# Kernel optimization log

Measured on AMD Instinct MI355X. Metric: run time of the kernel, lower is better.

## Reference

```python
import jax, jax.numpy as jnp
import numpy as np
import math

IN_DIM, OUT_DIM, NUM_BASIS = 256, 128, 6
MAX_IN_SEQ, MAX_OUT_SEQ = 512, 256
REDUCTION = 2
LN_EPS = 1e-5


def setup_inputs() -> dict:
    key = jax.random.key(0)
    ks = jax.random.split(key, 8)
    u = lambda k, shape, a: jax.random.uniform(k, shape, jnp.float32, -a, a)
    x = jax.random.normal(ks[0], (16, MAX_IN_SEQ, IN_DIM), jnp.float32)
    M = u(ks[1], (OUT_DIM, IN_DIM), 0.5)
    P = u(ks[2], (OUT_DIM, OUT_DIM, NUM_BASIS), 0.1)
    Linker = u(ks[3], (MAX_IN_SEQ, MAX_OUT_SEQ), 0.1)
    ln_gamma = jnp.ones((OUT_DIM,), jnp.float32)
    ln_beta = jnp.zeros((OUT_DIM,), jnp.float32)
    res_W = u(ks[4], (OUT_DIM, IN_DIM), 0.1)
    res_linker = u(ks[5], (MAX_IN_SEQ, MAX_OUT_SEQ), 0.1)
    # periods[i,j,g] = i*(out_dim*num_basis) + j*num_basis + g + 2 (non-trainable buffer)
    periods = (jnp.arange(OUT_DIM * OUT_DIM * NUM_BASIS, dtype=jnp.float32)
               .reshape(OUT_DIM, OUT_DIM, NUM_BASIS) + 2.0)
    return {"x": x, "M": M, "P": P, "Linker": Linker, "ln_gamma": ln_gamma,
            "ln_beta": ln_beta, "res_W": res_W, "res_linker": res_linker,
            "periods": periods, "actual_seq_len": 512}


def _layer_norm(z, gamma, beta):
    mu = jnp.mean(z, axis=-1, keepdims=True)
    var = jnp.var(z, axis=-1, keepdims=True)
    return (z - mu) * jax.lax.rsqrt(var + LN_EPS) * gamma + beta


def reference(x, M, P, Linker, ln_gamma, ln_beta, res_W, res_linker, periods, actual_seq_len):
    b, seq_len, _ = x.shape
    # Z = LN(x @ M^T)
    Z = _layer_norm(jnp.matmul(x, M.T), ln_gamma, ln_beta)  # (b, s, out)
    # position-dependent trig basis: phi[s,i,j,g] = cos(2*pi*s / periods[i,j,g])
    k = jnp.arange(seq_len, dtype=jnp.float32)[:, None, None, None]
    phi = jnp.cos(2.0 * math.pi * k / periods[None])          # (s, out, out, nb)
    # fold basis into per-position mixing matrix, then contract (matches sum over dims 3,4)
    W = jnp.einsum('ijg,sijg->sij', P, phi)                   # (s, out, out)
    T = jnp.einsum('bsj,sij->bsi', Z, W)                      # (b, s, out)
    # adaptive linker: reduce sequence length
    L = actual_seq_len
    Lo = max(1, L // REDUCTION)
    U = jnp.einsum('bsi,so->boi', T[:, :L], Linker[:L, :Lo])  # (b, out_seq, out)
    # 'separate' residual
    rfeat = jnp.matmul(x[:, :L], res_W.T)                     # (b, s, out)
    residual = jnp.einsum('bsi,so->boi', rfeat, res_linker[:L, :Lo])
    return U + residual
```

## Files before the change

kernel.cpp:

```cpp
#include <hip/hip_runtime.h>
#include <hip/hip_bf16.h>

#define LN_EPS 1e-5f


typedef __attribute__((ext_vector_type(8))) short short8;
typedef __attribute__((ext_vector_type(4))) float floatx4;

__device__ __forceinline__ unsigned short f2bf(float f) {
    __hip_bfloat16 h = __float2bfloat16(f);
    union { __hip_bfloat16 h; unsigned short u; } v; v.h = h; return v.u;
}
__device__ __forceinline__ unsigned int pack2(float a, float b) {
    return (unsigned int)f2bf(a) | ((unsigned int)f2bf(b) << 16);
}
__device__ __forceinline__ short8 pack8(float4 a, float4 b) {
    union { short8 s; uint4 u; } v;
    v.u.x = pack2(a.x, a.y); v.u.y = pack2(a.z, a.w);
    v.u.z = pack2(b.x, b.y); v.u.w = pack2(b.z, b.w);
    return v.s;
}

union SMem {
    struct { float buf[32 * 258]; float red1[256]; float red2[256]; float mus[32]; float rsg[32]; } p1;
    unsigned short lcat[32 * 260];
};

__global__ __launch_bounds__(256) void s1_produce(const float* __restrict__ x,
                                                  const float* __restrict__ M,
                                                  const float* __restrict__ resW,
                                                  const float* __restrict__ gamma,
                                                  const float* __restrict__ beta,
                                                  const float* __restrict__ P,
                                                  const float* __restrict__ periods,
                                                  const float* __restrict__ Linker,
                                                  const float* __restrict__ resL,
                                                  unsigned short* __restrict__ Z,
                                                  unsigned short* __restrict__ TRt,
                                                  unsigned short* __restrict__ W,
                                                  unsigned short* __restrict__ LcatT) {
    __shared__ SMem sm;
    int blk = blockIdx.x, t = threadIdx.x;
    int w = t >> 6, l = t & 63;
    int lane15 = l & 15, quad = l >> 4;

    if (blk < 512) {
        int et = blk & 31, sc = blk >> 5;
        int n0 = et * 512 + t * 2;
        int jj = n0 & 7, ii = (n0 >> 3) & 127, qd = (n0 >> 10) & 3, kq = n0 >> 12;
        int e0 = ii * 128 + kq * 32 + qd * 8 + jj;
        const float* pp = P + (size_t)e0 * 6;
        float4 pa = *(const float4*)(pp);
        float4 pb = *(const float4*)(pp + 4);
        float4 pc = *(const float4*)(pp + 8);
        float pf[12] = { pa.x, pa.y, pa.z, pa.w, pb.x, pb.y, pb.z, pb.w, pc.x, pc.y, pc.z, pc.w };
        const float* qp = periods + (size_t)e0 * 6;
        float4 qa = *(const float4*)(qp);
        float4 qb = *(const float4*)(qp + 4);
        float4 qc = *(const float4*)(qp + 8);
        float iv[12] = { __builtin_amdgcn_rcpf(qa.x), __builtin_amdgcn_rcpf(qa.y),
                         __builtin_amdgcn_rcpf(qa.z), __builtin_amdgcn_rcpf(qa.w),
                         __builtin_amdgcn_rcpf(qb.x), __builtin_amdgcn_rcpf(qb.y),
                         __builtin_amdgcn_rcpf(qb.z), __builtin_amdgcn_rcpf(qb.w),
                         __builtin_amdgcn_rcpf(qc.x), __builtin_amdgcn_rcpf(qc.y),
                         __builtin_amdgcn_rcpf(qc.z), __builtin_amdgcn_rcpf(qc.w) };
        float s0f = (float)(sc * 32);
        float tc[12], cm1[12], cc[12];
        #pragma unroll
        for (int g = 0; g < 12; ++g) {
            tc[g]  = 2.0f * __builtin_amdgcn_cosf(iv[g]);
            cm1[g] = __builtin_amdgcn_cosf(__builtin_amdgcn_fractf(s0f * iv[g]));
            cc[g]  = __builtin_amdgcn_cosf(__builtin_amdgcn_fractf((s0f + 1.0f) * iv[g]));
        }
        #pragma unroll 4
        for (int ss = 0; ss < 32; ++ss) {
            float a0 = 0.f, a1 = 0.f;
            #pragma unroll
            for (int g = 0; g < 6; ++g)  a0 += pf[g] * cm1[g];
            #pragma unroll
            for (int g = 6; g < 12; ++g) a1 += pf[g] * cm1[g];
            int s = sc * 32 + ss;
            *(unsigned int*)(W + (size_t)s * 16384 + n0) = pack2(a0, a1);
            #pragma unroll
            for (int g = 0; g < 12; ++g) {
                float cn = fmaf(tc[g], cc[g], -cm1[g]);
                cm1[g] = cc[g]; cc[g] = cn;
            }
        }
    } else if (blk < 768) {
        int r0 = (blk - 512) * 32;
        const float* wbase = (w < 2) ? M : resW;
        int wco = (w < 2) ? (w * 64) : (w * 64 - 128);
        floatx4 acc[2][4] = {};
        for (int kk = 0; kk < 256; kk += 32) {
            int k0 = kk + quad * 8;
            const float* xr0 = x + (size_t)(r0 + lane15) * 256 + k0;
            const float* xr1 = x + (size_t)(r0 + 16 + lane15) * 256 + k0;
            short8 a0 = pack8(*(const float4*)xr0, *(const float4*)(xr0 + 4));
            short8 a1 = pack8(*(const float4*)xr1, *(const float4*)(xr1 + 4));
            #pragma unroll
            for (int nt = 0; nt < 4; ++nt) {
                const float* br = wbase + (size_t)(wco + nt * 16 + lane15) * 256 + k0;
                short8 b = pack8(*(const float4*)br, *(const float4*)(br + 4));
                acc[0][nt] = __builtin_amdgcn_mfma_f32_16x16x32_bf16(a0, b, acc[0][nt], 0, 0, 0);
                acc[1][nt] = __builtin_amdgcn_mfma_f32_16x16x32_bf16(a1, b, acc[1][nt], 0, 0, 0);
            }
        }
        #pragma unroll
        for (int mt = 0; mt < 2; ++mt)
            #pragma unroll
            for (int nt = 0; nt < 4; ++nt)
                #pragma unroll
                for (int r = 0; r < 4; ++r) {
                    int ro = mt * 16 + quad * 4 + r;
                    int co = w * 64 + nt * 16 + lane15;
                    sm.p1.buf[ro * 258 + co] = acc[mt][nt][r];
                }
        __syncthreads();
        {
            int r = t >> 3, seg = t & 7;
            float s1 = 0.f, s2 = 0.f;
            #pragma unroll
            for (int e = 0; e < 16; ++e) { float v = sm.p1.buf[r * 258 + seg * 16 + e]; s1 += v; s2 += v * v; }
            sm.p1.red1[r * 8 + seg] = s1; sm.p1.red2[r * 8 + seg] = s2;
        }
        __syncthreads();
        if (t < 32) {
            float s1 = 0.f, s2 = 0.f;
            #pragma unroll
            for (int e = 0; e < 8; ++e) { s1 += sm.p1.red1[t * 8 + e]; s2 += sm.p1.red2[t * 8 + e]; }
            float mu = s1 * (1.0f / 128.0f);
            float var = s2 * (1.0f / 128.0f) - mu * mu;
            sm.p1.mus[t] = mu; sm.p1.rsg[t] = rsqrtf(var + LN_EPS);
        }
        __syncthreads();
        int b = r0 >> 9, s0 = r0 & 511;
        {
            int r = t >> 3, c0 = (t & 7) * 16;
            int s_t = s0 + r;
            float mu = sm.p1.mus[r], rs = sm.p1.rsg[r];
            float zv[16];
            #pragma unroll
            for (int e = 0; e < 16; ++e) {
                int j = c0 + e;
                zv[e] = (sm.p1.buf[r * 258 + j] - mu) * rs * gamma[j] + beta[j];
            }
            uint4 oz0, oz1;
            oz0.x = pack2(zv[0], zv[1]);  oz0.y = pack2(zv[2], zv[3]);
            oz0.z = pack2(zv[4], zv[5]);  oz0.w = pack2(zv[6], zv[7]);
            oz1.x = pack2(zv[8], zv[9]);  oz1.y = pack2(zv[10], zv[11]);
            oz1.z = pack2(zv[12], zv[13]); oz1.w = pack2(zv[14], zv[15]);
            unsigned short* zdst = Z + (size_t)s_t * 2048 + (((c0 >> 3) * 16 + b) << 3);
            *(uint4*)(zdst) = oz0;
            *(uint4*)(zdst + 128) = oz1;
        }
        {
            int j = t >> 1, sh = (t & 1) * 16;
            unsigned int ow[8];
            #pragma unroll
            for (int p = 0; p < 8; ++p) {
                float v0 = sm.p1.buf[(sh + 2 * p) * 258 + 128 + j];
                float v1 = sm.p1.buf[(sh + 2 * p + 1) * 258 + 128 + j];
                ow[p] = pack2(v0, v1);
            }
            int kqA = 64 + ((s0 + sh) >> 3);
            unsigned short* dst = TRt + (size_t)b * 131072 + ((size_t)(kqA * 128 + j) << 3);
            uint4 u0; u0.x = ow[0]; u0.y = ow[1]; u0.z = ow[2]; u0.w = ow[3];
            uint4 u1; u1.x = ow[4]; u1.y = ow[5]; u1.z = ow[6]; u1.w = ow[7];
            *(uint4*)(dst) = u0;
            *(uint4*)(dst + 1024) = u1;
        }
    } else {
        int kb = blk - 768;
        int k0 = kb * 32;
        const float* src = (kb < 16) ? (Linker + (size_t)k0 * 256)
                                     : (resL + (size_t)(k0 - 512) * 256);
        #pragma unroll
        for (int q = 0; q < 8; ++q) {
            int lin = t + 256 * q;
            int row = lin >> 6, col4 = (lin & 63) * 4;
            float4 v = *(const float4*)(src + row * 256 + col4);
            *(unsigned int*)(sm.lcat + row * 260 + col4)     = pack2(v.x, v.y);
            *(unsigned int*)(sm.lcat + row * 260 + col4 + 2) = pack2(v.z, v.w);
        }
        __syncthreads();
        int o = t;
        unsigned int outw[16];
        #pragma unroll
        for (int kp = 0; kp < 16; ++kp) {
            unsigned int lo = sm.lcat[(2 * kp) * 260 + o];
            unsigned int hi = sm.lcat[(2 * kp + 1) * 260 + o];
            outw[kp] = lo | (hi << 16);
        }
        #pragma unroll
        for (int qq = 0; qq < 4; ++qq) {
            uint4 u; u.x = outw[qq*4]; u.y = outw[qq*4+1]; u.z = outw[qq*4+2]; u.w = outw[qq*4+3];
            *(uint4*)(LcatT + (((size_t)(kb * 4 + qq) * 256 + o) << 3)) = u;
        }
    }
}

__global__ __launch_bounds__(256) void k2b_t(const unsigned short* __restrict__ W,
                                             const unsigned short* __restrict__ Z,
                                             unsigned short* __restrict__ TRt) {
    __shared__ unsigned short tbuf[16 * 64 * 4];
    int t = threadIdx.x, w = t >> 6, l = t & 63;
    int lane15 = l & 15, quad = l >> 4;
    int st = blockIdx.x >> 1, ih = blockIdx.x & 1;
    int s0 = st * 4;
    int i0 = ih * 64 + w * 16;
    #pragma unroll
    for (int ss = 0; ss < 4; ++ss) {
        int s = s0 + ss;
        floatx4 acc = {};
        #pragma unroll
        for (int kk = 0; kk < 4; ++kk) {
            int k0 = kk * 32 + quad * 8;
            short8 a  = *(const short8*)(Z + (size_t)s * 2048 + (((k0 >> 3) * 16 + lane15) << 3));
            short8 bf = *(const short8*)(W + (size_t)s * 16384 + (((k0 >> 3) * 128 + i0 + lane15) << 3));
            acc = __builtin_amdgcn_mfma_f32_16x16x32_bf16(a, bf, acc, 0, 0, 0);
        }
        int il = w * 16 + lane15;
        #pragma unroll
        for (int r = 0; r < 4; ++r) {
            int brow = quad * 4 + r;
            tbuf[(brow * 64 + il) * 4 + ss] = f2bf(acc[r]);
        }
    }
    __syncthreads();
    int ihb = ih * 64;
    #pragma unroll
    for (int q = 0; q < 4; ++q) {
        int p = t + 256 * q;
        int b = p >> 6, il = p & 63;
        uint2 v = *(const uint2*)(tbuf + p * 4);
        *(uint2*)(TRt + (size_t)b * 131072 + (((s0 >> 3) * 128 + ihb + il) << 3) + (s0 & 7)) = v;
    }
}

__global__ __launch_bounds__(256) void k3_out(const unsigned short* __restrict__ LcatT,
                                              const unsigned short* __restrict__ TRt,
                                              float* __restrict__ out) {
    __shared__ float red[4 * 32 * 64];
    int t = threadIdx.x, w = t >> 6, l = t & 63;
    int lane15 = l & 15, quad = l >> 4;
    int b = blockIdx.x, o0 = blockIdx.y * 32, i0 = blockIdx.z * 64;
    const unsigned short* trb = TRt + (size_t)b * 131072;
    floatx4 acc[2][4] = {};
    #pragma unroll 2
    for (int kk = 0; kk < 8; ++kk) {
        int k0 = w * 256 + kk * 32 + quad * 8;
        int kq = k0 >> 3;
        short8 afr0 = *(const short8*)(LcatT + (((size_t)kq * 256 + o0 + lane15) << 3));
        short8 afr1 = *(const short8*)(LcatT + (((size_t)kq * 256 + o0 + 16 + lane15) << 3));
        #pragma unroll
        for (int nt = 0; nt < 4; ++nt) {
            short8 bfr = *(const short8*)(trb + (((size_t)kq * 128 + i0 + nt * 16 + lane15) << 3));
            acc[0][nt] = __builtin_amdgcn_mfma_f32_16x16x32_bf16(afr0, bfr, acc[0][nt], 0, 0, 0);
            acc[1][nt] = __builtin_amdgcn_mfma_f32_16x16x32_bf16(afr1, bfr, acc[1][nt], 0, 0, 0);
        }
    }
    #pragma unroll
    for (int mt = 0; mt < 2; ++mt)
        #pragma unroll
        for (int nt = 0; nt < 4; ++nt)
            #pragma unroll
            for (int r = 0; r < 4; ++r) {
                int ro = mt * 16 + quad * 4 + r;
                int co = nt * 16 + lane15;
                red[(w * 32 + ro) * 64 + co] = acc[mt][nt][r];
            }
    __syncthreads();
    {
        int ro = t >> 3, c0 = (t & 7) * 8;
        float vs[8];
        #pragma unroll
        for (int e = 0; e < 8; ++e) {
            float sum = 0.f;
            #pragma unroll
            for (int ww = 0; ww < 4; ++ww) sum += red[(ww * 32 + ro) * 64 + c0 + e];
            vs[e] = sum;
        }
        float4 o1 = { vs[0], vs[1], vs[2], vs[3] };
        float4 o2 = { vs[4], vs[5], vs[6], vs[7] };
        size_t ob = ((size_t)b * 256 + o0 + ro) * 128 + i0 + c0;
        *(float4*)(out + ob) = o1;
        *(float4*)(out + ob + 4) = o2;
    }
}

extern "C" void kernel_launch(void* const* d_in, const int* in_sizes, int n_in,
                              void* d_out, int out_size, void* d_ws, size_t ws_size,
                              hipStream_t stream) {
    const float* x      = (const float*)d_in[0];
    const float* M      = (const float*)d_in[1];
    const float* P      = (const float*)d_in[2];
    const float* Linker = (const float*)d_in[3];
    const float* gamma  = (const float*)d_in[4];
    const float* beta   = (const float*)d_in[5];
    const float* resW   = (const float*)d_in[6];
    const float* resL   = (const float*)d_in[7];
    const float* periods= (const float*)d_in[8];
    (void)in_sizes; (void)n_in; (void)out_size; (void)ws_size;

    float* ws = (float*)d_ws;
    unsigned short* LcatT = (unsigned short*)(ws);
    unsigned short* Z     = (unsigned short*)(ws + 131072);
    unsigned short* TRt   = (unsigned short*)(ws + 655360);
    unsigned short* W     = (unsigned short*)(ws + 1703936);

    s1_produce<<<800, 256, 0, stream>>>(x, M, resW, gamma, beta, P, periods,
                                        Linker, resL, Z, TRt, W, LcatT);
    k2b_t<<<256, 256, 0, stream>>>(W, Z, TRt);
    k3_out<<<dim3(16, 8, 2), 256, 0, stream>>>(LcatT, TRt, (float*)d_out);
}
```

Before: 112.3 us.

## Stage x/M/resW tiles in LDS and reorder W layout for i-grouped MFMA reads

The projection GEMM now loads each k-slice of x and the concatenated M/resW weights once per block into padded LDS as bf16, instead of every wave reading and converting global rows itself. The layout of the precomputed per-position W matrix is changed so the 16 rows of an i-group sit in one contiguous block, and the producer and the k2b_t consumer index it consistently. Both changes aim to cut redundant global traffic and make the k2b_t loads more contiguous. The cost is two barriers per k-step and extra LDS use in the staged GEMM.

```diff
diff --git a/kernel.cpp b/kernel.cpp
--- a/kernel.cpp
+++ b/kernel.cpp
@@ -23,6 +23,7 @@
 
 union SMem {
     struct { float buf[32 * 258]; float red1[256]; float red2[256]; float mus[32]; float rsg[32]; } p1;
+    struct { unsigned short axs[32 * 40]; unsigned short bs[256 * 40]; } stg;
     unsigned short lcat[32 * 260];
 };
 
@@ -47,8 +48,8 @@
     if (blk < 512) {
         int et = blk & 31, sc = blk >> 5;
         int n0 = et * 512 + t * 2;
-        int jj = n0 & 7, ii = (n0 >> 3) & 127, qd = (n0 >> 10) & 3, kq = n0 >> 12;
-        int e0 = ii * 128 + kq * 32 + qd * 8 + jj;
+        int jj = n0 & 7, il = (n0 >> 3) & 15, kq = (n0 >> 7) & 15, ig = (n0 >> 11) & 7;
+        int e0 = (ig * 16 + il) * 128 + kq * 8 + jj;
         const float* pp = P + (size_t)e0 * 6;
         float4 pa = *(const float4*)(pp);
         float4 pb = *(const float4*)(pp + 4);
@@ -89,22 +90,36 @@
         }
     } else if (blk < 768) {
         int r0 = (blk - 512) * 32;
-        const float* wbase = (w < 2) ? M : resW;
-        int wco = (w < 2) ? (w * 64) : (w * 64 - 128);
+        int wco = w * 64;
         floatx4 acc[2][4] = {};
-        for (int kk = 0; kk < 256; kk += 32) {
-            int k0 = kk + quad * 8;
-            const float* xr0 = x + (size_t)(r0 + lane15) * 256 + k0;
-            const float* xr1 = x + (size_t)(r0 + 16 + lane15) * 256 + k0;
-            short8 a0 = pack8(*(const float4*)xr0, *(const float4*)(xr0 + 4));
-            short8 a1 = pack8(*(const float4*)xr1, *(const float4*)(xr1 + 4));
+        for (int km = 0; km < 256; km += 32) {
+            {
+                int row = t >> 3, c4 = (t & 7) * 4;
+                float4 v = *(const float4*)(x + (size_t)(r0 + row) * 256 + km + c4);
+                uint2 u; u.x = pack2(v.x, v.y); u.y = pack2(v.z, v.w);
+                *(uint2*)(sm.stg.axs + row * 40 + c4) = u;
+            }
+            #pragma unroll
+            for (int q = 0; q < 8; ++q) {
+                int idx = t + 256 * q;
+                int row = idx >> 3, c4 = (idx & 7) * 4;
+                const float* src = (row < 128) ? (M + (size_t)row * 256)
+                                               : (resW + (size_t)(row - 128) * 256);
+                float4 v = *(const float4*)(src + km + c4);
+                uint2 u; u.x = pack2(v.x, v.y); u.y = pack2(v.z, v.w);
+                *(uint2*)(sm.stg.bs + row * 40 + c4) = u;
+            }
+            __syncthreads();
+            int k0 = quad * 8;
+            short8 a0 = *(const short8*)(sm.stg.axs + lane15 * 40 + k0);
+            short8 a1 = *(const short8*)(sm.stg.axs + (16 + lane15) * 40 + k0);
             #pragma unroll
             for (int nt = 0; nt < 4; ++nt) {
-                const float* br = wbase + (size_t)(wco + nt * 16 + lane15) * 256 + k0;
-                short8 b = pack8(*(const float4*)br, *(const float4*)(br + 4));
+                short8 b = *(const short8*)(sm.stg.bs + (wco + nt * 16 + lane15) * 40 + k0);
                 acc[0][nt] = __builtin_amdgcn_mfma_f32_16x16x32_bf16(a0, b, acc[0][nt], 0, 0, 0);
                 acc[1][nt] = __builtin_amdgcn_mfma_f32_16x16x32_bf16(a1, b, acc[1][nt], 0, 0, 0);
             }
+            __syncthreads();
         }
         #pragma unroll
         for (int mt = 0; mt < 2; ++mt)
@@ -208,16 +223,16 @@
     int lane15 = l & 15, quad = l >> 4;
     int st = blockIdx.x >> 1, ih = blockIdx.x & 1;
     int s0 = st * 4;
-    int i0 = ih * 64 + w * 16;
+    int ig = ih * 4 + w;
     #pragma unroll
     for (int ss = 0; ss < 4; ++ss) {
         int s = s0 + ss;
         floatx4 acc = {};
         #pragma unroll
         for (int kk = 0; kk < 4; ++kk) {
-            int k0 = kk * 32 + quad * 8;
-            short8 a  = *(const short8*)(Z + (size_t)s * 2048 + (((k0 >> 3) * 16 + lane15) << 3));
-            short8 bf = *(const short8*)(W + (size_t)s * 16384 + (((k0 >> 3) * 128 + i0 + lane15) << 3));
+            int kq = kk * 4 + quad;
+            short8 a  = *(const short8*)(Z + (size_t)s * 2048 + ((kq * 16 + lane15) << 3));
+            short8 bf = *(const short8*)(W + (size_t)s * 16384 + (((ig * 16 + kq) * 16 + lane15) << 3));
             acc = __builtin_amdgcn_mfma_f32_16x16x32_bf16(a, bf, acc, 0, 0, 0);
         }
         int il = w * 16 + lane15;
```

Result: faster. 106.8 us (-4.9%).
